# Optimization experiments

Measured on AMD Instinct MI355X. Metric: run time of the kernel, lower is better.

The kernel has to match this reference:

```python
import jax, jax.numpy as jnp
import numpy as np


def _psf2otf(psf, shape):
    """Pad psf to `shape`, circularly shift so kernel center is at (0,0), FFT2."""
    pad = np.zeros(shape, dtype=np.float64)
    pad[: psf.shape[0], : psf.shape[1]] = psf
    for ax, k in enumerate(psf.shape):
        pad = np.roll(pad, -(k // 2), axis=ax)
    return np.fft.fft2(pad)


def setup_inputs() -> dict:
    key = jax.random.key(0)
    B, C, H, W = 32, 3, 512, 512
    output = jax.random.normal(key, (B, C, H, W), dtype=jnp.float32)
    return {"output": output}


def reference(output) -> jnp.ndarray:
    B, C, H, W = output.shape
    # Frequency-domain gradient filters (static, computed at trace time).
    fx = jnp.asarray(_psf2otf(np.array([[-1.0, 1.0]]), (H, W)), dtype=jnp.complex64)
    fy = jnp.asarray(_psf2otf(np.array([[-1.0], [1.0]]), (H, W)), dtype=jnp.complex64)
    # One batched FFT over (B, C, H, W) instead of B*C separate fft2 calls.
    F = jnp.fft.fft2(output)            # (B, C, H, W) complex64
    gx = jnp.fft.ifft2(F * fx)          # horizontal gradient (complex)
    gy = jnp.fft.ifft2(F * fy)          # vertical gradient (complex)
    # torch.norm over the stacked (gx, gy) dim of complex values = sqrt(|gx|^2 + |gy|^2)
    mag = jnp.sqrt(jnp.abs(gx) ** 2 + jnp.abs(gy) ** 2)
    denom = jnp.asarray(B * C * H * W, dtype=mag.dtype)
    return jnp.sum(mag) / denom
```

## Files before the change

### kernel.cpp

```cpp
#include <hip/hip_runtime.h>


#define DIM_H 512
#define DIM_W 512
#define PLANES 96
#define TOTAL (PLANES * DIM_H * DIM_W)
#define NV (TOTAL / 4)
#define NBLOCKS 2048
#define NTHREADS 256

__global__ __launch_bounds__(NTHREADS) void tv_partial(const float* __restrict__ in,
                                                       float* __restrict__ partial) {
    const float4* __restrict__ in4 = (const float4*)in;
    int tid = blockIdx.x * NTHREADS + threadIdx.x;
    float s = 0.0f;

    for (int i = tid; i < NV; i += NBLOCKS * NTHREADS) {
        int p  = i >> 16;
        int r  = i & 65535;
        int y  = r >> 7;
        int x4 = r & 127;

        float4 c = in4[i];

        int ydn = (y + 1) & (DIM_H - 1);
        float4 d = in4[(p << 16) | (ydn << 7) | x4];

        int xw = ((x4 << 2) + 4) & (DIM_W - 1);
        float e = in[(p << 18) + (y << 9) + xw];

        float dx0 = c.x - c.y, dy0 = c.x - d.x;
        float dx1 = c.y - c.z, dy1 = c.y - d.y;
        float dx2 = c.z - c.w, dy2 = c.z - d.z;
        float dx3 = c.w - e,   dy3 = c.w - d.w;

        s += sqrtf(dx0 * dx0 + dy0 * dy0);
        s += sqrtf(dx1 * dx1 + dy1 * dy1);
        s += sqrtf(dx2 * dx2 + dy2 * dy2);
        s += sqrtf(dx3 * dx3 + dy3 * dy3);
    }

    #pragma unroll
    for (int off = 32; off > 0; off >>= 1)
        s += __shfl_down(s, off, 64);

    __shared__ float smem[NTHREADS / 64];
    int lane = threadIdx.x & 63;
    int wave = threadIdx.x >> 6;
    if (lane == 0) smem[wave] = s;
    __syncthreads();
    if (threadIdx.x == 0)
        partial[blockIdx.x] = smem[0] + smem[1] + smem[2] + smem[3];
}

__global__ __launch_bounds__(256) void tv_final(const float* __restrict__ partial,
                                                float* __restrict__ out) {
    float s = 0.0f;
    for (int i = threadIdx.x; i < NBLOCKS; i += 256)
        s += partial[i];

    #pragma unroll
    for (int off = 32; off > 0; off >>= 1)
        s += __shfl_down(s, off, 64);

    __shared__ float smem[4];
    int lane = threadIdx.x & 63;
    int wave = threadIdx.x >> 6;
    if (lane == 0) smem[wave] = s;
    __syncthreads();
    if (threadIdx.x == 0)
        out[0] = (smem[0] + smem[1] + smem[2] + smem[3]) * (1.0f / (float)TOTAL);
}

extern "C" void kernel_launch(void* const* d_in, const int* in_sizes, int n_in,
                              void* d_out, int out_size, void* d_ws, size_t ws_size,
                              hipStream_t stream) {
    const float* in = (const float*)d_in[0];
    float* out = (float*)d_out;
    float* partial = (float*)d_ws;

    tv_partial<<<NBLOCKS, NTHREADS, 0, stream>>>(in, partial);
    tv_final<<<1, 256, 0, stream>>>(partial, out);
}
```

Measured before the change: 144.8 us.

## Stage row tiles plus halo in LDS via direct global-to-LDS loads

Each block now owns a 16-row slice of one plane. It loads that slice plus one halo row straight into shared memory with global_load_lds, so the vertical neighbour is read from LDS instead of being fetched a second time from global memory. The horizontal neighbour comes from a wave shuffle rather than an extra scalar load. The cost is a shared-memory tile of about 35KB per block, a barrier before compute, and no grid-stride loop, since the block count is now planes × slices.

```diff
diff --git a/kernel.cpp b/kernel.cpp
--- a/kernel.cpp
+++ b/kernel.cpp
@@ -5,51 +5,87 @@
 #define DIM_W 512
 #define PLANES 96
 #define TOTAL (PLANES * DIM_H * DIM_W)
-#define NV (TOTAL / 4)
-#define NBLOCKS 2048
+#define W4 128
+#define ROWS 16
+#define SLICES (DIM_H / ROWS)
 #define NTHREADS 256
+#define NBLOCKS (PLANES * SLICES)
+#define TILE_F4 ((ROWS + 1) * W4)
 
-__global__ __launch_bounds__(NTHREADS) void tv_partial(const float* __restrict__ in,
-                                                       float* __restrict__ partial) {
+__global__ __launch_bounds__(NTHREADS, 4) void tv_partial(const float* __restrict__ in,
+                                                          float* __restrict__ partial) {
+    __shared__ float4 tile[TILE_F4];
+    __shared__ float smem[NTHREADS / 64];
+
+    const int t    = threadIdx.x;
+    const int lane = t & 63;
+    const int w    = t >> 6;
+    const int p    = blockIdx.x >> 5;
+    const int k    = blockIdx.x & (SLICES - 1);
+
+    const int gbase = (p << 16) + (k << 11);
+    const int hbase = (k == SLICES - 1) ? (p << 16) : (gbase + ROWS * W4);
+
     const float4* __restrict__ in4 = (const float4*)in;
-    int tid = blockIdx.x * NTHREADS + threadIdx.x;
+
+    #pragma unroll
+    for (int j = 0; j < 8; ++j) {
+        __builtin_amdgcn_global_load_lds(
+            (const __attribute__((address_space(1))) void*)(in4 + gbase + j * 256 + t),
+            (__attribute__((address_space(3))) void*)(tile + j * 256 + w * 64),
+            16, 0, 0);
+    }
+    if (w < 2) {
+        __builtin_amdgcn_global_load_lds(
+            (const __attribute__((address_space(1))) void*)(in4 + hbase + w * 64 + lane),
+            (__attribute__((address_space(3))) void*)(tile + 2048 + w * 64),
+            16, 0, 0);
+    }
+    __syncthreads();
+
+    const int src = (lane + 1) & 63;
+    const bool last = (lane == 63);
     float s = 0.0f;
 
-    for (int i = tid; i < NV; i += NBLOCKS * NTHREADS) {
-        int p  = i >> 16;
-        int r  = i & 65535;
-        int y  = r >> 7;
-        int x4 = r & 127;
+    int r0 = w << 2;
+    float4 A = tile[(r0 << 7) + lane];
+    float4 B = tile[(r0 << 7) + 64 + lane];
 
-        float4 c = in4[i];
+#define TV_ROW(A_, B_, DA_, DB_)                                                 \
+    do {                                                                         \
+        float n0 = __shfl((A_).x, src, 64);                                      \
+        float n1 = __shfl((B_).x, src, 64);                                      \
+        float e0 = last ? n1 : n0;         \
+        float e1 = last ? n0 : n1;             \
+        float tt;                                                                \
+        tt = (A_).x - (A_).y; s += sqrtf(tt*tt + ((A_).x-(DA_).x)*((A_).x-(DA_).x)); \
+        tt = (A_).y - (A_).z; s += sqrtf(tt*tt + ((A_).y-(DA_).y)*((A_).y-(DA_).y)); \
+        tt = (A_).z - (A_).w; s += sqrtf(tt*tt + ((A_).z-(DA_).z)*((A_).z-(DA_).z)); \
+        tt = (A_).w - e0;     s += sqrtf(tt*tt + ((A_).w-(DA_).w)*((A_).w-(DA_).w)); \
+        tt = (B_).x - (B_).y; s += sqrtf(tt*tt + ((B_).x-(DB_).x)*((B_).x-(DB_).x)); \
+        tt = (B_).y - (B_).z; s += sqrtf(tt*tt + ((B_).y-(DB_).y)*((B_).y-(DB_).y)); \
+        tt = (B_).z - (B_).w; s += sqrtf(tt*tt + ((B_).z-(DB_).z)*((B_).z-(DB_).z)); \
+        tt = (B_).w - e1;     s += sqrtf(tt*tt + ((B_).w-(DB_).w)*((B_).w-(DB_).w)); \
+    } while (0)
 
-        int ydn = (y + 1) & (DIM_H - 1);
-        float4 d = in4[(p << 16) | (ydn << 7) | x4];
-
-        int xw = ((x4 << 2) + 4) & (DIM_W - 1);
-        float e = in[(p << 18) + (y << 9) + xw];
-
-        float dx0 = c.x - c.y, dy0 = c.x - d.x;
-        float dx1 = c.y - c.z, dy1 = c.y - d.y;
-        float dx2 = c.z - c.w, dy2 = c.z - d.z;
-        float dx3 = c.w - e,   dy3 = c.w - d.w;
-
-        s += sqrtf(dx0 * dx0 + dy0 * dy0);
-        s += sqrtf(dx1 * dx1 + dy1 * dy1);
-        s += sqrtf(dx2 * dx2 + dy2 * dy2);
-        s += sqrtf(dx3 * dx3 + dy3 * dy3);
+    #pragma unroll
+    for (int j = 1; j <= 4; ++j) {
+        int rn = r0 + j;
+        float4 DA = tile[(rn << 7) + lane];
+        float4 DB = tile[(rn << 7) + 64 + lane];
+        TV_ROW(A, B, DA, DB);
+        A = DA;
+        B = DB;
     }
+#undef TV_ROW
 
     #pragma unroll
     for (int off = 32; off > 0; off >>= 1)
         s += __shfl_down(s, off, 64);
 
-    __shared__ float smem[NTHREADS / 64];
-    int lane = threadIdx.x & 63;
-    int wave = threadIdx.x >> 6;
-    if (lane == 0) smem[wave] = s;
+    if (lane == 0) smem[w] = s;
     __syncthreads();
-    if (threadIdx.x == 0)
+    if (t == 0)
         partial[blockIdx.x] = smem[0] + smem[1] + smem[2] + smem[3];
 }
 
```

Measured after the change: 146.3 us. No clear change (+1.0%).
